# Kernel optimization log

Hardware: AMD Instinct MI355X
Metric: run time of the kernel (lower is better)

The kernel has to match this reference:

```python
import jax, jax.numpy as jnp
import numpy as np

N = 100000
IN_CH = 128
OUT_CH = 40
K = 2
E = 3200000


def setup_inputs() -> dict:
    key = jax.random.key(0)
    k1, k2, k3, k4 = jax.random.split(key, 4)
    x = jax.random.normal(k1, (N, IN_CH), dtype=jnp.float32)
    edge_index = jax.random.randint(k2, (2, E), 0, N, dtype=jnp.int64)
    # Linear params (PyG Linear: glorot-style init approximated)
    scale = 1.0 / np.sqrt(IN_CH)
    W = jax.random.uniform(k3, (IN_CH, OUT_CH), dtype=jnp.float32, minval=-scale, maxval=scale)
    b = jax.random.uniform(k4, (OUT_CH,), dtype=jnp.float32, minval=-scale, maxval=scale)
    return {"x": x, "edge_index": edge_index, "W": W, "b": b}


def reference(x, edge_index, W, b):
    n = x.shape[0]
    row, col = edge_index[0], edge_index[1]  # source -> target
    # gcn_norm: add self loops, symmetric normalization
    loop = jnp.arange(n, dtype=row.dtype)
    row = jnp.concatenate([row, loop])
    col = jnp.concatenate([col, loop])
    ones = jnp.ones(row.shape[0], dtype=x.dtype)
    deg = jax.ops.segment_sum(ones, col, num_segments=n)  # in-degree incl. self-loop
    deg_inv_sqrt = jnp.where(deg > 0, jax.lax.rsqrt(deg), 0.0)
    norm = deg_inv_sqrt[row] * deg_inv_sqrt[col]  # [E+N]
    h = x
    for _ in range(K):
        # sparse SpMM: out[col] += norm * h[row]
        h = jax.ops.segment_sum(norm[:, None] * h[row], col, num_segments=n)
    logits = h @ W + b
    return jax.nn.log_softmax(logits, axis=-1)
```

## Files before the change

### kernel.cpp

```cpp
#include <hip/hip_runtime.h>
#include <hip/hip_fp16.h>
#include <math.h>

#define NN 100000
#define ICH 128
#define OCH 40
#define NE 3200000
#define BSH 8
#define BNODES 256
#define BMASK 255
#define NB 391
#define CAP 9216
#define TILE 4096
#define NBIN ((NE + TILE - 1) / TILE)
#define YSTRIDE 40
#define YU2 (YSTRIDE / 8)

typedef __attribute__((ext_vector_type(2))) float floatx2;
typedef __attribute__((ext_vector_type(4))) float floatx4;

__device__ __forceinline__ void acc_fp8x8(const uint2 u, float* acc) {
    floatx2 p0 = __builtin_amdgcn_cvt_pk_f32_fp8((int)u.x, false);
    floatx2 p1 = __builtin_amdgcn_cvt_pk_f32_fp8((int)u.x, true);
    floatx2 p2 = __builtin_amdgcn_cvt_pk_f32_fp8((int)u.y, false);
    floatx2 p3 = __builtin_amdgcn_cvt_pk_f32_fp8((int)u.y, true);
    acc[0] += p0.x; acc[1] += p0.y; acc[2] += p1.x; acc[3] += p1.y;
    acc[4] += p2.x; acc[5] += p2.y; acc[6] += p3.x; acc[7] += p3.y;
}

__device__ __forceinline__ uint2 pack_fp8x8(const float* v) {
    int lo = 0, hi = 0;
    lo = __builtin_amdgcn_cvt_pk_fp8_f32(v[0], v[1], lo, false);
    lo = __builtin_amdgcn_cvt_pk_fp8_f32(v[2], v[3], lo, true);
    hi = __builtin_amdgcn_cvt_pk_fp8_f32(v[4], v[5], hi, false);
    hi = __builtin_amdgcn_cvt_pk_fp8_f32(v[6], v[7], hi, true);
    return make_uint2((unsigned int)lo, (unsigned int)hi);
}

__device__ __forceinline__ void row_gather(const int* __restrict__ csr, int kb, int ke, int q,
                                           const uint2* __restrict__ base, float* acc) {
    int k = kb;
    if (k + 8 <= ke) {
        int s[8];
        uint2 v[8];
#pragma unroll
        for (int j = 0; j < 8; ++j) s[j] = csr[k + j];
#pragma unroll
        for (int j = 0; j < 8; ++j) v[j] = base[(size_t)s[j] * YU2 + q];
        k += 8;
        for (; k + 8 <= ke; k += 8) {
            int s2[8];
            uint2 w[8];
#pragma unroll
            for (int j = 0; j < 8; ++j) s2[j] = csr[k + j];
#pragma unroll
            for (int j = 0; j < 8; ++j) w[j] = base[(size_t)s2[j] * YU2 + q];
#pragma unroll
            for (int j = 0; j < 8; ++j) acc_fp8x8(v[j], acc);
#pragma unroll
            for (int j = 0; j < 8; ++j) v[j] = w[j];
        }
#pragma unroll
        for (int j = 0; j < 8; ++j) acc_fp8x8(v[j], acc);
    }
    for (; k < ke; ++k) acc_fp8x8(base[(size_t)csr[k] * YU2 + q], acc);
}

__global__ __launch_bounds__(512) void k_bin(const int* __restrict__ ei, int* __restrict__ bcursor,
                                             unsigned int* __restrict__ packed) {
    __shared__ unsigned int entries[TILE];
    __shared__ unsigned short bid[TILE];
    __shared__ int hist[512], base[512], gbase[512], cur[512];
    int t = threadIdx.x;
    int tile0 = blockIdx.x * TILE;
    int tcnt = min(TILE, NE - tile0);
    hist[t] = 0;
    __syncthreads();
    int src[8], dst[8];
#pragma unroll
    for (int i = 0; i < 8; ++i) {
        int l = t + i * 512;
        if (l < tcnt) {
            int e = tile0 + l;
            src[i] = ei[e];
            dst[i] = ei[NE + e];
            atomicAdd(&hist[dst[i] >> BSH], 1);
        } else dst[i] = -1;
    }
    __syncthreads();
    int own = hist[t];
    base[t] = own;
    __syncthreads();
    for (int off = 1; off < 512; off <<= 1) {
        int v = (t >= off) ? base[t - off] : 0;
        __syncthreads();
        base[t] += v;
        __syncthreads();
    }
    int excl = base[t] - own;
    __syncthreads();
    base[t] = excl;
    cur[t] = excl;
    if (t < NB && own > 0) gbase[t] = atomicAdd(&bcursor[t], own);
    __syncthreads();
#pragma unroll
    for (int i = 0; i < 8; ++i) {
        if (dst[i] >= 0) {
            int bb = dst[i] >> BSH;
            int pos = atomicAdd(&cur[bb], 1);
            entries[pos] = ((unsigned int)(dst[i] & BMASK) << 17) | (unsigned int)src[i];
            bid[pos] = (unsigned short)bb;
        }
    }
    __syncthreads();
    for (int l = t; l < tcnt; l += 512) {
        int bb = bid[l];
        packed[(size_t)bb * CAP + gbase[bb] + (l - base[bb])] = entries[l];
    }
}

__global__ __launch_bounds__(512) void k_bscan(const int* __restrict__ bcursor, int* __restrict__ bbase,
                                               int* __restrict__ rowptr) {
    __shared__ int s[512];
    int t = threadIdx.x;
    int v = (t < NB) ? bcursor[t] : 0;
    s[t] = v;
    __syncthreads();
    for (int off = 1; off < 512; off <<= 1) {
        int u = (t >= off) ? s[t - off] : 0;
        __syncthreads();
        s[t] += u;
        __syncthreads();
    }
    if (t < NB) bbase[t] = s[t] - v;
    if (t == 0) rowptr[NN] = NE;
}

__global__ __launch_bounds__(512) void k_csr(const int* __restrict__ bcursor, const int* __restrict__ bbase,
                                             const unsigned int* __restrict__ packed,
                                             int* __restrict__ rowptr, float* __restrict__ dis,
                                             int* __restrict__ csr) {
    __shared__ unsigned int ent[CAP];
    __shared__ int hist[BNODES], cur[BNODES], ps[BNODES];
    int b = blockIdx.x;
    int t = threadIdx.x;
    int cnt = bcursor[b];
    int cbase = bbase[b];
    int node0 = b << BSH;
    int nn = min(BNODES, NN - node0);
    if (t < BNODES) hist[t] = 0;
    __syncthreads();
    const unsigned int* pk = packed + (size_t)b * CAP;
    for (int l = t; l < cnt; l += 512) {
        unsigned int e = pk[l];
        ent[l] = e;
        atomicAdd(&hist[e >> 17], 1);
    }
    __syncthreads();
    if (t < BNODES) ps[t] = hist[t];
    __syncthreads();
    for (int off = 1; off < BNODES; off <<= 1) {
        int u = (t >= off && t < BNODES) ? ps[t - off] : 0;
        __syncthreads();
        if (t < BNODES) ps[t] += u;
        __syncthreads();
    }
    if (t < BNODES) {
        int excl = ps[t] - hist[t];
        cur[t] = excl;
        if (t < nn) {
            rowptr[node0 + t] = cbase + excl;
            dis[node0 + t] = rsqrtf((float)hist[t] + 1.0f);
        }
    }
    __syncthreads();
    for (int l = t; l < cnt; l += 512) {
        unsigned int e = ent[l];
        int pos = atomicAdd(&cur[e >> 17], 1);
        csr[cbase + pos] = (int)(e & 0x1FFFF);
    }
}

__global__ __launch_bounds__(256) void k_xw(const float* __restrict__ x, const float* __restrict__ W,
                                            const float* __restrict__ dis, unsigned char* __restrict__ y0) {
    __shared__ float Wl[ICH * OCH];
    int t = threadIdx.x;
    {
        const float4* W4 = (const float4*)W;
        float4* Wl4 = (float4*)Wl;
#pragma unroll
        for (int i = 0; i < 5; ++i) Wl4[t + 256 * i] = W4[t + 256 * i];
    }
    __syncthreads();
    int row = blockIdx.x * 256 + t;
    if (row >= NN) return;
    const float4* xr = (const float4*)(x + (size_t)row * ICH);
    float acc[OCH];
#pragma unroll
    for (int c = 0; c < OCH; ++c) acc[c] = 0.f;
    for (int k4 = 0; k4 < ICH / 4; ++k4) {
        float4 xv = xr[k4];
        const float4* wr4 = (const float4*)(Wl + (size_t)(4 * k4) * OCH);
#pragma unroll
        for (int c4 = 0; c4 < 10; ++c4) {
            float4 w0 = wr4[c4];
            float4 w1 = wr4[10 + c4];
            float4 w2 = wr4[20 + c4];
            float4 w3 = wr4[30 + c4];
            acc[4 * c4 + 0] += xv.x * w0.x + xv.y * w1.x + xv.z * w2.x + xv.w * w3.x;
            acc[4 * c4 + 1] += xv.x * w0.y + xv.y * w1.y + xv.z * w2.y + xv.w * w3.y;
            acc[4 * c4 + 2] += xv.x * w0.z + xv.y * w1.z + xv.z * w2.z + xv.w * w3.z;
            acc[4 * c4 + 3] += xv.x * w0.w + xv.y * w1.w + xv.z * w2.w + xv.w * w3.w;
        }
    }
    float d = dis[row];
#pragma unroll
    for (int c = 0; c < OCH; ++c) acc[c] *= d;
    uint2* yr = (uint2*)(y0 + (size_t)row * YSTRIDE);
#pragma unroll
    for (int q = 0; q < 5; ++q) yr[q] = pack_fp8x8(acc + 8 * q);
}

__global__ __launch_bounds__(256) void k_hop1(const int* __restrict__ rowptr, const int* __restrict__ csr,
                                              const float* __restrict__ dis, const unsigned char* __restrict__ y0,
                                              unsigned char* __restrict__ y1) {
    int g = blockIdx.x * 256 + threadIdx.x;
    if (g >= NN * 5) return;
    int i = g / 5, q = g - 5 * i;
    const uint2* base = (const uint2*)y0;
    float acc[8];
#pragma unroll
    for (int j = 0; j < 8; ++j) acc[j] = 0.f;
    acc_fp8x8(base[(size_t)i * YU2 + q], acc);
    row_gather(csr, rowptr[i], rowptr[i + 1], q, base, acc);
    float d = dis[i], d2 = d * d;
#pragma unroll
    for (int j = 0; j < 8; ++j) acc[j] *= d2;
    ((uint2*)y1)[(size_t)i * YU2 + q] = pack_fp8x8(acc);
}

__global__ __launch_bounds__(320) void k_hop2f(const int* __restrict__ rowptr, const int* __restrict__ csr,
                                               const float* __restrict__ dis, const unsigned char* __restrict__ y1,
                                               const float* __restrict__ b, float* __restrict__ out) {
    __shared__ float red[64][5];
    int tid = threadIdx.x;
    int lg = tid / 5;
    int q = tid - 5 * lg;
    int g = blockIdx.x * 64 + lg;
    bool active = (g < NN);
    float l[8];
    if (active) {
        const uint2* base = (const uint2*)y1;
        float acc[8];
#pragma unroll
        for (int j = 0; j < 8; ++j) acc[j] = 0.f;
        acc_fp8x8(base[(size_t)g * YU2 + q], acc);
        row_gather(csr, rowptr[g], rowptr[g + 1], q, base, acc);
        float d = dis[g];
#pragma unroll
        for (int j = 0; j < 8; ++j) l[j] = d * acc[j] + b[8 * q + j];
    } else {
#pragma unroll
        for (int j = 0; j < 8; ++j) l[j] = -1e30f;
    }
    float m8 = l[0];
#pragma unroll
    for (int j = 1; j < 8; ++j) m8 = fmaxf(m8, l[j]);
    red[lg][q] = m8;
    __syncthreads();
    float gm = red[lg][0];
#pragma unroll
    for (int j = 1; j < 5; ++j) gm = fmaxf(gm, red[lg][j]);
    __syncthreads();
    float s8 = 0.f;
#pragma unroll
    for (int j = 0; j < 8; ++j) s8 += __expf(l[j] - gm);
    red[lg][q] = s8;
    __syncthreads();
    float gs = red[lg][0];
#pragma unroll
    for (int j = 1; j < 5; ++j) gs += red[lg][j];
    float ls = __logf(gs) + gm;
    if (active) {
        floatx4* orow = (floatx4*)(out + (size_t)g * OCH + 8 * q);
        floatx4 o0 = {l[0] - ls, l[1] - ls, l[2] - ls, l[3] - ls};
        floatx4 o1 = {l[4] - ls, l[5] - ls, l[6] - ls, l[7] - ls};
        __builtin_nontemporal_store(o0, orow);
        __builtin_nontemporal_store(o1, orow + 1);
    }
}

extern "C" void kernel_launch(void* const* d_in, const int* in_sizes, int n_in,
                              void* d_out, int out_size, void* d_ws, size_t ws_size,
                              hipStream_t stream) {
    const float* x  = (const float*)d_in[0];
    const int*   ei = (const int*)d_in[1];
    const float* W  = (const float*)d_in[2];
    const float* b  = (const float*)d_in[3];
    float* out = (float*)d_out;

    char* ws = (char*)d_ws;
    int*           bcursor = (int*)(ws + 0);
    int*           bbase   = (int*)(ws + 2048);
    int*           rowptr  = (int*)(ws + 4096);
    float*         dis     = (float*)(ws + 409600);
    unsigned int*  packed  = (unsigned int*)(ws + 819200);
    unsigned char* y0      = (unsigned char*)(ws + 819200);
    unsigned char* y1      = (unsigned char*)(ws + 4822016);
    int*           csr     = (int*)(ws + 15239168);

    hipMemsetAsync(bcursor, 0, NB * sizeof(int), stream);
    k_bin<<<NBIN, 512, 0, stream>>>(ei, bcursor, packed);
    k_bscan<<<1, 512, 0, stream>>>(bcursor, bbase, rowptr);
    k_csr<<<NB, 512, 0, stream>>>(bcursor, bbase, packed, rowptr, dis, csr);
    k_xw<<<(NN + 255) / 256, 256, 0, stream>>>(x, W, dis, y0);
    k_hop1<<<(NN * 5 + 255) / 256, 256, 0, stream>>>(rowptr, csr, dis, y0, y1);
    k_hop2f<<<(NN + 63) / 64, 320, 0, stream>>>(rowptr, csr, dis, y1, b, out);
}
```

Baseline: 252.3 us.

## Compute X·W with split-bf16 MFMA using W pre-packed in the scan kernel

Moves the dense 128x40 projection from per-thread FP32 FMA loops onto MFMA 16x16x32 bf16 instructions. Each wave handles 16-row tiles, and precision is kept with a three-product hi/lo split (ah·whi + al·whi + ah·wlo). W is converted once inside the single-block scan kernel into an MFMA-ready hi/lo bf16 fragment layout in workspace, and each wave loads it into registers. The trade-off is byte-granular scattered fp8 stores instead of packed uint2 stores, extra conversion work on x, and a shifted workspace layout.

```diff
diff --git a/kernel.cpp b/kernel.cpp
--- a/kernel.cpp
+++ b/kernel.cpp
@@ -15,9 +15,17 @@
 #define NBIN ((NE + TILE - 1) / TILE)
 #define YSTRIDE 40
 #define YU2 (YSTRIDE / 8)
+#define XWBLK 1563
 
 typedef __attribute__((ext_vector_type(2))) float floatx2;
 typedef __attribute__((ext_vector_type(4))) float floatx4;
+typedef __attribute__((ext_vector_type(8))) short bf16x8;
+
+__device__ __forceinline__ unsigned int pk_bf16(float a, float b) {
+    unsigned int r;
+    asm("v_cvt_pk_bf16_f32 %0, %1, %2" : "=v"(r) : "v"(a), "v"(b));
+    return r;
+}
 
 __device__ __forceinline__ void acc_fp8x8(const uint2 u, float* acc) {
     floatx2 p0 = __builtin_amdgcn_cvt_pk_f32_fp8((int)u.x, false);
@@ -120,7 +128,8 @@
 }
 
 __global__ __launch_bounds__(512) void k_bscan(const int* __restrict__ bcursor, int* __restrict__ bbase,
-                                               int* __restrict__ rowptr) {
+                                               int* __restrict__ rowptr, const float* __restrict__ W,
+                                               unsigned int* __restrict__ wbf) {
     __shared__ int s[512];
     int t = threadIdx.x;
     int v = (t < NB) ? bcursor[t] : 0;
@@ -134,6 +143,31 @@
     }
     if (t < NB) bbase[t] = s[t] - v;
     if (t == 0) rowptr[NN] = NE;
+    for (int e = t; e < 1536; e += 512) {
+        int hs = e / 768;
+        int rem = e - hs * 768;
+        int ss = rem / 192;
+        int rem2 = rem - ss * 192;
+        int n = rem2 >> 6;
+        int lane = rem2 & 63;
+        int kbase = ss * 32 + (lane >> 4) * 8;
+        int col = n * 16 + (lane & 15);
+        unsigned int u4[4];
+#pragma unroll
+        for (int p = 0; p < 4; ++p) {
+            float f0 = (col < OCH) ? W[(size_t)(kbase + 2 * p) * OCH + col] : 0.f;
+            float f1 = (col < OCH) ? W[(size_t)(kbase + 2 * p + 1) * OCH + col] : 0.f;
+            unsigned int h = pk_bf16(f0, f1);
+            if (hs == 0) {
+                u4[p] = h;
+            } else {
+                float l0 = f0 - __uint_as_float(h << 16);
+                float l1 = f1 - __uint_as_float(h & 0xFFFF0000u);
+                u4[p] = pk_bf16(l0, l1);
+            }
+        }
+        ((uint4*)wbf)[e] = make_uint4(u4[0], u4[1], u4[2], u4[3]);
+    }
 }
 
 __global__ __launch_bounds__(512) void k_csr(const int* __restrict__ bcursor, const int* __restrict__ bbase,
@@ -181,44 +215,74 @@
     }
 }
 
-__global__ __launch_bounds__(256) void k_xw(const float* __restrict__ x, const float* __restrict__ W,
+__global__ __launch_bounds__(128) void k_xw(const float* __restrict__ x, const unsigned int* __restrict__ wbf,
                                             const float* __restrict__ dis, unsigned char* __restrict__ y0) {
-    __shared__ float Wl[ICH * OCH];
     int t = threadIdx.x;
-    {
-        const float4* W4 = (const float4*)W;
-        float4* Wl4 = (float4*)Wl;
-#pragma unroll
-        for (int i = 0; i < 5; ++i) Wl4[t + 256 * i] = W4[t + 256 * i];
-    }
-    __syncthreads();
-    int row = blockIdx.x * 256 + t;
-    if (row >= NN) return;
-    const float4* xr = (const float4*)(x + (size_t)row * ICH);
-    float acc[OCH];
-#pragma unroll
-    for (int c = 0; c < OCH; ++c) acc[c] = 0.f;
-    for (int k4 = 0; k4 < ICH / 4; ++k4) {
-        float4 xv = xr[k4];
-        const float4* wr4 = (const float4*)(Wl + (size_t)(4 * k4) * OCH);
-#pragma unroll
-        for (int c4 = 0; c4 < 10; ++c4) {
-            float4 w0 = wr4[c4];
-            float4 w1 = wr4[10 + c4];
-            float4 w2 = wr4[20 + c4];
-            float4 w3 = wr4[30 + c4];
-            acc[4 * c4 + 0] += xv.x * w0.x + xv.y * w1.x + xv.z * w2.x + xv.w * w3.x;
-            acc[4 * c4 + 1] += xv.x * w0.y + xv.y * w1.y + xv.z * w2.y + xv.w * w3.y;
-            acc[4 * c4 + 2] += xv.x * w0.z + xv.y * w1.z + xv.z * w2.z + xv.w * w3.z;
-            acc[4 * c4 + 3] += xv.x * w0.w + xv.y * w1.w + xv.z * w2.w + xv.w * w3.w;
-        }
-    }
-    float d = dis[row];
-#pragma unroll
-    for (int c = 0; c < OCH; ++c) acc[c] *= d;
-    uint2* yr = (uint2*)(y0 + (size_t)row * YSTRIDE);
-#pragma unroll
-    for (int q = 0; q < 5; ++q) yr[q] = pack_fp8x8(acc + 8 * q);
+    int wid = t >> 6, lane = t & 63;
+    const bf16x8* wf = (const bf16x8*)wbf;
+    bf16x8 whi[4][3], wlo[4][3];
+#pragma unroll
+    for (int s = 0; s < 4; ++s)
+#pragma unroll
+        for (int n = 0; n < 3; ++n) {
+            whi[s][n] = wf[(s * 3 + n) * 64 + lane];
+            wlo[s][n] = wf[768 / 1 * 0 + (768) + 0 * 64 - 768 + (1 * 768) + (s * 3 + n) * 64 + lane];
+        }
+    int rbase = blockIdx.x * 64 + wid * 32;
+#pragma unroll
+    for (int tt = 0; tt < 2; ++tt) {
+        int r0 = rbase + tt * 16;
+        int rowa = r0 + (lane & 15);
+        int rowc = min(rowa, NN - 1);
+        int kb = (lane >> 4) * 8;
+        const float4* xp = (const float4*)(x + (size_t)rowc * ICH + kb);
+        float4 xa[4][2];
+#pragma unroll
+        for (int s = 0; s < 4; ++s) {
+            xa[s][0] = xp[s * 8];
+            xa[s][1] = xp[s * 8 + 1];
+        }
+        floatx4 acc[3] = {{0.f, 0.f, 0.f, 0.f}, {0.f, 0.f, 0.f, 0.f}, {0.f, 0.f, 0.f, 0.f}};
+#pragma unroll
+        for (int s = 0; s < 4; ++s) {
+            float f[8] = {xa[s][0].x, xa[s][0].y, xa[s][0].z, xa[s][0].w,
+                          xa[s][1].x, xa[s][1].y, xa[s][1].z, xa[s][1].w};
+            union { unsigned int u[4]; bf16x8 v; } ah, al;
+#pragma unroll
+            for (int p = 0; p < 4; ++p) {
+                unsigned int h = pk_bf16(f[2 * p], f[2 * p + 1]);
+                ah.u[p] = h;
+                float l0 = f[2 * p] - __uint_as_float(h << 16);
+                float l1 = f[2 * p + 1] - __uint_as_float(h & 0xFFFF0000u);
+                al.u[p] = pk_bf16(l0, l1);
+            }
+#pragma unroll
+            for (int n = 0; n < 3; ++n) {
+                acc[n] = __builtin_amdgcn_mfma_f32_16x16x32_bf16(ah.v, whi[s][n], acc[n], 0, 0, 0);
+                acc[n] = __builtin_amdgcn_mfma_f32_16x16x32_bf16(al.v, whi[s][n], acc[n], 0, 0, 0);
+                acc[n] = __builtin_amdgcn_mfma_f32_16x16x32_bf16(ah.v, wlo[s][n], acc[n], 0, 0, 0);
+            }
+        }
+        int rc0 = r0 + (lane >> 4) * 4;
+        float dd[4];
+#pragma unroll
+        for (int r = 0; r < 4; ++r) dd[r] = (rc0 + r < NN) ? dis[rc0 + r] : 0.f;
+#pragma unroll
+        for (int n = 0; n < 3; ++n) {
+            int col = n * 16 + (lane & 15);
+            if (col < OCH) {
+#pragma unroll
+                for (int r = 0; r < 4; ++r) {
+                    int row = rc0 + r;
+                    if (row < NN) {
+                        float val = acc[n][r] * dd[r];
+                        int p8 = __builtin_amdgcn_cvt_pk_fp8_f32(val, val, 0, false);
+                        y0[(size_t)row * YSTRIDE + col] = (unsigned char)(p8 & 0xFF);
+                    }
+                }
+            }
+        }
+    }
 }
 
 __global__ __launch_bounds__(256) void k_hop1(const int* __restrict__ rowptr, const int* __restrict__ csr,
@@ -304,16 +368,17 @@
     int*           bbase   = (int*)(ws + 2048);
     int*           rowptr  = (int*)(ws + 4096);
     float*         dis     = (float*)(ws + 409600);
-    unsigned int*  packed  = (unsigned int*)(ws + 819200);
-    unsigned char* y0      = (unsigned char*)(ws + 819200);
-    unsigned char* y1      = (unsigned char*)(ws + 4822016);
-    int*           csr     = (int*)(ws + 15239168);
+    unsigned int*  wbf     = (unsigned int*)(ws + 811008);
+    unsigned int*  packed  = (unsigned int*)(ws + 843776);
+    unsigned char* y0      = (unsigned char*)(ws + 843776);
+    unsigned char* y1      = (unsigned char*)(ws + 4849664);
+    int*           csr     = (int*)(ws + 15261696);
 
     hipMemsetAsync(bcursor, 0, NB * sizeof(int), stream);
     k_bin<<<NBIN, 512, 0, stream>>>(ei, bcursor, packed);
-    k_bscan<<<1, 512, 0, stream>>>(bcursor, bbase, rowptr);
+    k_bscan<<<1, 512, 0, stream>>>(bcursor, bbase, rowptr, W, wbf);
     k_csr<<<NB, 512, 0, stream>>>(bcursor, bbase, packed, rowptr, dis, csr);
-    k_xw<<<(NN + 255) / 256, 256, 0, stream>>>(x, W, dis, y0);
+    k_xw<<<XWBLK, 128, 0, stream>>>(x, wbf, dis, y0);
     k_hop1<<<(NN * 5 + 255) / 256, 256, 0, stream>>>(rowptr, csr, dis, y0, y1);
     k_hop2f<<<(NN + 63) / 64, 320, 0, stream>>>(rowptr, csr, dis, y1, b, out);
 }
```

After: 245.5 us. 1.03x faster.
